# Kernel optimization log

Hardware: AMD Instinct MI355X
Metric: run time of the kernel (lower is better)

The kernel has to match this reference:

```python
import jax, jax.numpy as jnp
import numpy as np

TEMPERATURE = 2.0  # registered buffer in the torch module
TAU = 1.0
N_HEADS = 16


def setup_inputs() -> dict:
    key = jax.random.key(0)
    ks = jax.random.split(key, 8)
    B, S, D, N = 4, 1024, 1024, 4096
    scale = 1.0 / np.sqrt(D)
    return {
        "x": jax.random.normal(ks[0], (B, S, D), jnp.float32),
        "in_proj_w": jax.random.normal(ks[1], (3 * D, D), jnp.float32) * scale,
        "in_proj_b": jnp.zeros((3 * D,), jnp.float32),
        "out_w": jax.random.normal(ks[2], (D, D), jnp.float32) * scale,
        "out_b": jnp.zeros((D,), jnp.float32),
        "aff_w": jax.random.normal(ks[3], (N, D), jnp.float32) * scale,
        "aff_b": jnp.zeros((N,), jnp.float32),
        "k": 256,
    }


def _forward(x, in_proj_w, in_proj_b, out_w, out_b, aff_w, aff_b, k):
    B, S, D = x.shape
    H = N_HEADS
    hd = D // H
    # packed QKV projection (torch nn.MultiheadAttention layout)
    qkv = x @ in_proj_w.T + in_proj_b                      # [B,S,3D]
    q, kk, v = jnp.split(qkv, 3, axis=-1)
    q = q.reshape(B, S, H, hd).transpose(0, 2, 1, 3)       # [B,H,S,hd]
    kk = kk.reshape(B, S, H, hd).transpose(0, 2, 1, 3)
    v = v.reshape(B, S, H, hd).transpose(0, 2, 1, 3)
    scores = jnp.einsum("bhqd,bhkd->bhqk", q, kk) / np.sqrt(hd)
    attn = jax.nn.softmax(scores, axis=-1)                 # [B,H,S,S]
    ctx = jnp.einsum("bhqk,bhkd->bhqd", attn, v)
    ctx = ctx.transpose(0, 2, 1, 3).reshape(B, S, D)
    context = ctx @ out_w.T + out_b                        # [B,S,D]
    # neuron affinity -> max-pool over sequence
    affinity = context @ aff_w.T + aff_b                   # [B,S,N]
    pooled = affinity.max(axis=1)                          # [B,N]
    logits = pooled / TEMPERATURE
    # eval path of gumbel-softmax-topk: plain softmax(logits / tau)
    soft = jax.nn.softmax(logits / TAU, axis=-1)
    _, idx = jax.lax.top_k(logits, k)                      # [B,k]
    mask = jnp.zeros_like(soft).at[jnp.arange(soft.shape[0])[:, None], idx].set(1.0)
    masked = soft * mask
    weights = masked / (masked.sum(axis=-1, keepdims=True) + 1e-8)
    return idx, weights, context


def reference(x, in_proj_w, in_proj_b, out_w, out_b, aff_w, aff_b, k):
    return _forward(x, in_proj_w, in_proj_b, out_w, out_b, aff_w, aff_b, k)
```

## Files before the change

### kernel.cpp

```cpp
#include <hip/hip_runtime.h>
#include <math.h>

namespace {

constexpr int Bb = 4, Ss = 1024, Dd = 1024, Hh = 16, HDim = 64, Nn = 4096;
constexpr int Mm = Bb * Ss;

template <bool AFFMAX>
__global__ __launch_bounds__(256) void gemm_kernel(
    const float* __restrict__ A, const float* __restrict__ W,
    const float* __restrict__ bias, float* __restrict__ C, int K, int lda,
    int ldw, int ldc) {
  __shared__ float As[16][128];
  __shared__ float Ws[16][128];
  const int tid = threadIdx.x;
  const int tx = tid & 15, ty = tid >> 4;
  const int n0 = blockIdx.x * 128, m0 = blockIdx.y * 128;
  const int r = tid >> 1, kc = (tid & 1) * 8;
  const float* Arow = A + (size_t)(m0 + r) * lda + kc;
  const float* Wrow = W + (size_t)(n0 + r) * ldw + kc;
  float acc[8][8] = {};
  for (int kt = 0; kt < K; kt += 16) {
    float4 a0 = *(const float4*)(Arow + kt);
    float4 a1 = *(const float4*)(Arow + kt + 4);
    float4 w0 = *(const float4*)(Wrow + kt);
    float4 w1 = *(const float4*)(Wrow + kt + 4);
    __syncthreads();
    As[kc + 0][r] = a0.x; As[kc + 1][r] = a0.y;
    As[kc + 2][r] = a0.z; As[kc + 3][r] = a0.w;
    As[kc + 4][r] = a1.x; As[kc + 5][r] = a1.y;
    As[kc + 6][r] = a1.z; As[kc + 7][r] = a1.w;
    Ws[kc + 0][r] = w0.x; Ws[kc + 1][r] = w0.y;
    Ws[kc + 2][r] = w0.z; Ws[kc + 3][r] = w0.w;
    Ws[kc + 4][r] = w1.x; Ws[kc + 5][r] = w1.y;
    Ws[kc + 6][r] = w1.z; Ws[kc + 7][r] = w1.w;
    __syncthreads();
#pragma unroll
    for (int kk = 0; kk < 16; ++kk) {
      float4 a0r = *(const float4*)&As[kk][ty * 8];
      float4 a1r = *(const float4*)&As[kk][ty * 8 + 4];
      float4 b0r = *(const float4*)&Ws[kk][tx * 8];
      float4 b1r = *(const float4*)&Ws[kk][tx * 8 + 4];
      float av[8] = {a0r.x, a0r.y, a0r.z, a0r.w, a1r.x, a1r.y, a1r.z, a1r.w};
      float bv[8] = {b0r.x, b0r.y, b0r.z, b0r.w, b1r.x, b1r.y, b1r.z, b1r.w};
#pragma unroll
      for (int i = 0; i < 8; ++i)
#pragma unroll
        for (int j = 0; j < 8; ++j)
          acc[i][j] = fmaf(av[i], bv[j], acc[i][j]);
    }
  }
  if constexpr (!AFFMAX) {
#pragma unroll
    for (int i = 0; i < 8; ++i) {
      const int row = m0 + ty * 8 + i;
      float* crow = C + (size_t)row * ldc + n0 + tx * 8;
#pragma unroll
      for (int j = 0; j < 8; ++j) crow[j] = acc[i][j] + bias[n0 + tx * 8 + j];
    }
  } else {
    float cm[8];
#pragma unroll
    for (int j = 0; j < 8; ++j) {
      float m = acc[0][j];
#pragma unroll
      for (int i = 1; i < 8; ++i) m = fmaxf(m, acc[i][j]);
      cm[j] = m;
    }
    __syncthreads();
#pragma unroll
    for (int j = 0; j < 8; ++j) As[ty][tx * 8 + j] = cm[j];
    __syncthreads();
    if (tid < 128) {
      float m = As[0][tid];
#pragma unroll
      for (int yy = 1; yy < 16; ++yy) m = fmaxf(m, As[yy][tid]);
      C[(size_t)blockIdx.y * ldc + n0 + tid] = m;
    }
  }
}

__global__ __launch_bounds__(256) void attn_kernel(
    const float* __restrict__ qkv, float* __restrict__ ctx) {
  constexpr int LD = 68;
  __shared__ float Qs[64][LD];
  __shared__ float KPs[64][LD];
  __shared__ float Vs[64][LD];
  const int tid = threadIdx.x;
  const int tx = tid & 15, ty = tid >> 4;
  const int bh = blockIdx.y, b = bh >> 4, h = bh & 15;
  const int q0 = blockIdx.x * 64;
  const size_t rowstride = 3 * Dd;
  const float* qbase = qkv + (size_t)b * Ss * rowstride + h * HDim;
  const float* kbase = qbase + Dd;
  const float* vbase = qbase + 2 * Dd;
  {
    const int r = tid >> 2, c0 = (tid & 3) * 16;
    const float* qr = qbase + (size_t)(q0 + r) * rowstride + c0;
#pragma unroll
    for (int c = 0; c < 16; c += 4)
      *(float4*)&Qs[r][c0 + c] = *(const float4*)(qr + c);
  }
  float O[4][4] = {};
  float mrow[4] = {-INFINITY, -INFINITY, -INFINITY, -INFINITY};
  float lrow[4] = {};
  for (int kt0 = 0; kt0 < Ss; kt0 += 64) {
    const int r = tid >> 2, c0 = (tid & 3) * 16;
    const float* kr = kbase + (size_t)(kt0 + r) * rowstride + c0;
    const float* vr = vbase + (size_t)(kt0 + r) * rowstride + c0;
    float4 kv[4], vv[4];
#pragma unroll
    for (int c = 0; c < 4; ++c) {
      kv[c] = *(const float4*)(kr + c * 4);
      vv[c] = *(const float4*)(vr + c * 4);
    }
    __syncthreads();
#pragma unroll
    for (int c = 0; c < 4; ++c) {
      *(float4*)&Vs[r][c0 + 4 * c] = vv[c];
      KPs[c0 + 4 * c + 0][r] = kv[c].x;
      KPs[c0 + 4 * c + 1][r] = kv[c].y;
      KPs[c0 + 4 * c + 2][r] = kv[c].z;
      KPs[c0 + 4 * c + 3][r] = kv[c].w;
    }
    __syncthreads();
    float sc[4][4] = {};
#pragma unroll
    for (int d0 = 0; d0 < HDim; d0 += 4) {
      float4 qa[4];
#pragma unroll
      for (int i = 0; i < 4; ++i) qa[i] = *(const float4*)&Qs[ty * 4 + i][d0];
#pragma unroll
      for (int dd = 0; dd < 4; ++dd) {
        float4 kb = *(const float4*)&KPs[d0 + dd][tx * 4];
#pragma unroll
        for (int i = 0; i < 4; ++i) {
          float q = (dd == 0) ? qa[i].x : (dd == 1) ? qa[i].y
                    : (dd == 2) ? qa[i].z : qa[i].w;
          sc[i][0] = fmaf(q, kb.x, sc[i][0]);
          sc[i][1] = fmaf(q, kb.y, sc[i][1]);
          sc[i][2] = fmaf(q, kb.z, sc[i][2]);
          sc[i][3] = fmaf(q, kb.w, sc[i][3]);
        }
      }
    }
    __syncthreads();
#pragma unroll
    for (int i = 0; i < 4; ++i) {
      float s0 = sc[i][0] * 0.125f, s1 = sc[i][1] * 0.125f;
      float s2 = sc[i][2] * 0.125f, s3 = sc[i][3] * 0.125f;
      float tm = fmaxf(fmaxf(s0, s1), fmaxf(s2, s3));
#pragma unroll
      for (int msk = 1; msk < 16; msk <<= 1) tm = fmaxf(tm, __shfl_xor(tm, msk));
      float mnew = fmaxf(mrow[i], tm);
      float p0 = expf(s0 - mnew), p1 = expf(s1 - mnew);
      float p2 = expf(s2 - mnew), p3 = expf(s3 - mnew);
      KPs[ty * 4 + i][tx * 4 + 0] = p0;
      KPs[ty * 4 + i][tx * 4 + 1] = p1;
      KPs[ty * 4 + i][tx * 4 + 2] = p2;
      KPs[ty * 4 + i][tx * 4 + 3] = p3;
      float rs = p0 + p1 + p2 + p3;
#pragma unroll
      for (int msk = 1; msk < 16; msk <<= 1) rs += __shfl_xor(rs, msk);
      float corr = expf(mrow[i] - mnew);
      lrow[i] = lrow[i] * corr + rs;
      mrow[i] = mnew;
      O[i][0] *= corr; O[i][1] *= corr; O[i][2] *= corr; O[i][3] *= corr;
    }
    __syncthreads();
#pragma unroll
    for (int j0 = 0; j0 < 64; j0 += 4) {
      float4 pa[4];
#pragma unroll
      for (int i = 0; i < 4; ++i) pa[i] = *(const float4*)&KPs[ty * 4 + i][j0];
#pragma unroll
      for (int jj = 0; jj < 4; ++jj) {
        float4 vb = *(const float4*)&Vs[j0 + jj][tx * 4];
#pragma unroll
        for (int i = 0; i < 4; ++i) {
          float p = (jj == 0) ? pa[i].x : (jj == 1) ? pa[i].y
                    : (jj == 2) ? pa[i].z : pa[i].w;
          O[i][0] = fmaf(p, vb.x, O[i][0]);
          O[i][1] = fmaf(p, vb.y, O[i][1]);
          O[i][2] = fmaf(p, vb.z, O[i][2]);
          O[i][3] = fmaf(p, vb.w, O[i][3]);
        }
      }
    }
  }
#pragma unroll
  for (int i = 0; i < 4; ++i) {
    float inv = 1.0f / lrow[i];
    const int srow = q0 + ty * 4 + i;
    float* orow = ctx + ((size_t)(b * Ss + srow)) * Dd + h * HDim + tx * 4;
    orow[0] = O[i][0] * inv;
    orow[1] = O[i][1] * inv;
    orow[2] = O[i][2] * inv;
    orow[3] = O[i][3] * inv;
  }
}

__device__ inline unsigned int f2s(float f) {
  unsigned int u = __float_as_uint(f);
  return (u >> 31) ? ~u : (u | 0x80000000u);
}
__device__ inline float s2f(unsigned int s) {
  unsigned int u = (s >> 31) ? (s & 0x7fffffffu) : ~s;
  return __uint_as_float(u);
}

__global__ __launch_bounds__(256) void router_kernel(
    const float* __restrict__ partial, const float* __restrict__ aff_b,
    const int* __restrict__ kp, float* __restrict__ out, int out_size) {
  __shared__ unsigned long long keys[Nn];
  __shared__ float lorig[Nn];
  __shared__ float rv[4];
  const int tid = threadIdx.x;
  const int b = blockIdx.x;
  const int kcount = *kp;
  float* idx_out = out;
  float* w_out = out + (out_size - Mm * Dd - Bb * Nn);
  for (int n = tid; n < Nn; n += 256) {
    float m = partial[(size_t)(b * 8) * Nn + n];
#pragma unroll
    for (int t = 1; t < 8; ++t)
      m = fmaxf(m, partial[(size_t)(b * 8 + t) * Nn + n]);
    float lg = (m + aff_b[n]) * 0.5f;
    lorig[n] = lg;
    keys[n] = ((unsigned long long)f2s(lg) << 32) |
              (unsigned int)(Nn - 1 - n);
  }
  __syncthreads();
  for (int kk = 2; kk <= Nn; kk <<= 1) {
    for (int j = kk >> 1; j > 0; j >>= 1) {
#pragma unroll 4
      for (int t = tid; t < Nn / 2; t += 256) {
        const int i = 2 * j * (t / j) + (t % j);
        const int p = i + j;
        const bool desc = ((i & kk) == 0);
        unsigned long long a = keys[i], c = keys[p];
        if (desc ? (a < c) : (a > c)) { keys[i] = c; keys[p] = a; }
      }
      __syncthreads();
    }
  }
  const float gm = s2f((unsigned int)(keys[0] >> 32));
  float se = 0.f;
  for (int n = tid; n < Nn; n += 256) se += expf(lorig[n] - gm);
#pragma unroll
  for (int msk = 1; msk < 64; msk <<= 1) se += __shfl_xor(se, msk);
  if ((tid & 63) == 0) rv[tid >> 6] = se;
  __syncthreads();
  se = rv[0] + rv[1] + rv[2] + rv[3];
  __syncthreads();
  float es = 0.f;
  for (int p = tid; p < kcount; p += 256)
    es += expf(s2f((unsigned int)(keys[p] >> 32)) - gm);
#pragma unroll
  for (int msk = 1; msk < 64; msk <<= 1) es += __shfl_xor(es, msk);
  if ((tid & 63) == 0) rv[tid >> 6] = es;
  __syncthreads();
  es = rv[0] + rv[1] + rv[2] + rv[3];
  const float wd = es / se + 1e-8f;
  for (int n = tid; n < Nn; n += 256) w_out[(size_t)b * Nn + n] = 0.f;
  __syncthreads();
  for (int p = tid; p < kcount; p += 256) {
    const unsigned long long kkey = keys[p];
    const int n = Nn - 1 - (int)(kkey & 0xffffffffu);
    const float val = s2f((unsigned int)(kkey >> 32));
    idx_out[b * kcount + p] = (float)n;
    w_out[(size_t)b * Nn + n] = (expf(val - gm) / se) / wd;
  }
}

}

extern "C" void kernel_launch(void* const* d_in, const int* in_sizes, int n_in,
                              void* d_out, int out_size, void* d_ws,
                              size_t ws_size, hipStream_t stream) {
  (void)in_sizes; (void)n_in; (void)ws_size;
  const float* x = (const float*)d_in[0];
  const float* in_proj_w = (const float*)d_in[1];
  const float* in_proj_b = (const float*)d_in[2];
  const float* out_w = (const float*)d_in[3];
  const float* out_b = (const float*)d_in[4];
  const float* aff_w = (const float*)d_in[5];
  const float* aff_b = (const float*)d_in[6];
  const int* kp = (const int*)d_in[7];

  float* qkv = (float*)d_ws;
  float* ctxws = qkv + (size_t)Mm * 3 * Dd;
  float* partial = ctxws + (size_t)Mm * Dd;

  float* out = (float*)d_out;
  float* ctx_out = out + ((size_t)out_size - (size_t)Mm * Dd);

  gemm_kernel<false><<<dim3(3 * Dd / 128, Mm / 128), 256, 0, stream>>>(
      x, in_proj_w, in_proj_b, qkv, Dd, Dd, Dd, 3 * Dd);
  attn_kernel<<<dim3(Ss / 64, Bb * Hh), 256, 0, stream>>>(qkv, ctxws);
  gemm_kernel<false><<<dim3(Dd / 128, Mm / 128), 256, 0, stream>>>(
      ctxws, out_w, out_b, ctx_out, Dd, Dd, Dd, Dd);
  gemm_kernel<true><<<dim3(Nn / 128, Mm / 128), 256, 0, stream>>>(
      ctx_out, aff_w, nullptr, partial, Dd, Dd, Dd, Nn);
  router_kernel<<<dim3(Bb), 256, 0, stream>>>(partial, aff_b, kp, out, out_size);
}
```

Baseline: 1.287 ms.

## Double-buffer GEMM tiles, swizzle attention LDS, prefetch K/V, vectorize stores

The FP32 GEMM now keeps two shared-memory tile buffers, loads the next K slice into registers while the current one is computed, and maps threads to a warp-tiled layout. The max-pool epilogue reduces with shuffles, and bias/output writes use float4. The attention kernel XOR-swizzles its Q/K/V/P shared-memory indices to cut bank conflicts, prefetches the next K/V tile into registers, and switches to the fast __expf intrinsic. Together these aim to hide global-load latency and raise LDS throughput, at the cost of more registers and slightly less accurate exponentials.

```diff
diff --git a/kernel.cpp b/kernel.cpp
--- a/kernel.cpp
+++ b/kernel.cpp
@@ -6,43 +6,66 @@
 constexpr int Bb = 4, Ss = 1024, Dd = 1024, Hh = 16, HDim = 64, Nn = 4096;
 constexpr int Mm = Bb * Ss;
 
-template <bool AFFMAX>
-__global__ __launch_bounds__(256) void gemm_kernel(
+template <int MODE>
+__global__ __launch_bounds__(256, 4) void gemm_f32(
     const float* __restrict__ A, const float* __restrict__ W,
-    const float* __restrict__ bias, float* __restrict__ C, int K, int lda,
-    int ldw, int ldc) {
-  __shared__ float As[16][128];
-  __shared__ float Ws[16][128];
+    const float* __restrict__ bias, float* __restrict__ C, const int K,
+    const int ldc) {
+  __shared__ float As[2][16][128];
+  __shared__ float Ws[2][16][128];
   const int tid = threadIdx.x;
-  const int tx = tid & 15, ty = tid >> 4;
-  const int n0 = blockIdx.x * 128, m0 = blockIdx.y * 128;
-  const int r = tid >> 1, kc = (tid & 1) * 8;
-  const float* Arow = A + (size_t)(m0 + r) * lda + kc;
-  const float* Wrow = W + (size_t)(n0 + r) * ldw + kc;
+  const int lane = tid & 63, wv = tid >> 6;
+  const int wm = wv >> 1, wn = wv & 1;
+  const int lty = lane >> 3, ltx = lane & 7;
+  const int m0 = blockIdx.y * 128, n0 = blockIdx.x * 128;
+  const int row0 = wm * 64 + lty * 8;
+  const int col0 = wn * 64 + ltx * 8;
+  const int srow = tid >> 1, shalf = tid & 1;
+  const float* Ap = A + (size_t)(m0 + srow) * K + shalf * 8;
+  const float* Wp = W + (size_t)(n0 + srow) * K + shalf * 8;
+
+  float4 ar0 = *(const float4*)(Ap);
+  float4 ar1 = *(const float4*)(Ap + 4);
+  float4 wr0 = *(const float4*)(Wp);
+  float4 wr1 = *(const float4*)(Wp + 4);
+
   float acc[8][8] = {};
-  for (int kt = 0; kt < K; kt += 16) {
-    float4 a0 = *(const float4*)(Arow + kt);
-    float4 a1 = *(const float4*)(Arow + kt + 4);
-    float4 w0 = *(const float4*)(Wrow + kt);
-    float4 w1 = *(const float4*)(Wrow + kt + 4);
-    __syncthreads();
-    As[kc + 0][r] = a0.x; As[kc + 1][r] = a0.y;
-    As[kc + 2][r] = a0.z; As[kc + 3][r] = a0.w;
-    As[kc + 4][r] = a1.x; As[kc + 5][r] = a1.y;
-    As[kc + 6][r] = a1.z; As[kc + 7][r] = a1.w;
-    Ws[kc + 0][r] = w0.x; Ws[kc + 1][r] = w0.y;
-    Ws[kc + 2][r] = w0.z; Ws[kc + 3][r] = w0.w;
-    Ws[kc + 4][r] = w1.x; Ws[kc + 5][r] = w1.y;
-    Ws[kc + 6][r] = w1.z; Ws[kc + 7][r] = w1.w;
+  const int NT = K / 16;
+#pragma unroll 1
+  for (int kt = 0; kt < NT; ++kt) {
+    const int cb = kt & 1;
+    As[cb][shalf * 8 + 0][srow] = ar0.x;
+    As[cb][shalf * 8 + 1][srow] = ar0.y;
+    As[cb][shalf * 8 + 2][srow] = ar0.z;
+    As[cb][shalf * 8 + 3][srow] = ar0.w;
+    As[cb][shalf * 8 + 4][srow] = ar1.x;
+    As[cb][shalf * 8 + 5][srow] = ar1.y;
+    As[cb][shalf * 8 + 6][srow] = ar1.z;
+    As[cb][shalf * 8 + 7][srow] = ar1.w;
+    Ws[cb][shalf * 8 + 0][srow] = wr0.x;
+    Ws[cb][shalf * 8 + 1][srow] = wr0.y;
+    Ws[cb][shalf * 8 + 2][srow] = wr0.z;
+    Ws[cb][shalf * 8 + 3][srow] = wr0.w;
+    Ws[cb][shalf * 8 + 4][srow] = wr1.x;
+    Ws[cb][shalf * 8 + 5][srow] = wr1.y;
+    Ws[cb][shalf * 8 + 6][srow] = wr1.z;
+    Ws[cb][shalf * 8 + 7][srow] = wr1.w;
+    if (kt + 1 < NT) {
+      const int kb = (kt + 1) * 16;
+      ar0 = *(const float4*)(Ap + kb);
+      ar1 = *(const float4*)(Ap + kb + 4);
+      wr0 = *(const float4*)(Wp + kb);
+      wr1 = *(const float4*)(Wp + kb + 4);
+    }
     __syncthreads();
 #pragma unroll
     for (int kk = 0; kk < 16; ++kk) {
-      float4 a0r = *(const float4*)&As[kk][ty * 8];
-      float4 a1r = *(const float4*)&As[kk][ty * 8 + 4];
-      float4 b0r = *(const float4*)&Ws[kk][tx * 8];
-      float4 b1r = *(const float4*)&Ws[kk][tx * 8 + 4];
-      float av[8] = {a0r.x, a0r.y, a0r.z, a0r.w, a1r.x, a1r.y, a1r.z, a1r.w};
-      float bv[8] = {b0r.x, b0r.y, b0r.z, b0r.w, b1r.x, b1r.y, b1r.z, b1r.w};
+      float4 a0 = *(const float4*)&As[cb][kk][row0];
+      float4 a1 = *(const float4*)&As[cb][kk][row0 + 4];
+      float4 b0 = *(const float4*)&Ws[cb][kk][col0];
+      float4 b1 = *(const float4*)&Ws[cb][kk][col0 + 4];
+      float av[8] = {a0.x, a0.y, a0.z, a0.w, a1.x, a1.y, a1.z, a1.w};
+      float bv[8] = {b0.x, b0.y, b0.z, b0.w, b1.x, b1.y, b1.z, b1.w};
 #pragma unroll
       for (int i = 0; i < 8; ++i)
 #pragma unroll
@@ -50,13 +73,20 @@
           acc[i][j] = fmaf(av[i], bv[j], acc[i][j]);
     }
   }
-  if constexpr (!AFFMAX) {
+
+  if constexpr (MODE == 0) {
+    float4 bb0 = *(const float4*)&bias[n0 + col0];
+    float4 bb1 = *(const float4*)&bias[n0 + col0 + 4];
+    const float bv[8] = {bb0.x, bb0.y, bb0.z, bb0.w, bb1.x, bb1.y, bb1.z, bb1.w};
 #pragma unroll
     for (int i = 0; i < 8; ++i) {
-      const int row = m0 + ty * 8 + i;
-      float* crow = C + (size_t)row * ldc + n0 + tx * 8;
-#pragma unroll
-      for (int j = 0; j < 8; ++j) crow[j] = acc[i][j] + bias[n0 + tx * 8 + j];
+      float* crow = C + (size_t)(m0 + row0 + i) * ldc + n0 + col0;
+      float4 o0 = {acc[i][0] + bv[0], acc[i][1] + bv[1], acc[i][2] + bv[2],
+                   acc[i][3] + bv[3]};
+      float4 o1 = {acc[i][4] + bv[4], acc[i][5] + bv[5], acc[i][6] + bv[6],
+                   acc[i][7] + bv[7]};
+      *(float4*)(crow) = o0;
+      *(float4*)(crow + 4) = o1;
     }
   } else {
     float cm[8];
@@ -65,18 +95,22 @@
       float m = acc[0][j];
 #pragma unroll
       for (int i = 1; i < 8; ++i) m = fmaxf(m, acc[i][j]);
+      m = fmaxf(m, __shfl_xor(m, 8));
+      m = fmaxf(m, __shfl_xor(m, 16));
+      m = fmaxf(m, __shfl_xor(m, 32));
       cm[j] = m;
     }
     __syncthreads();
-#pragma unroll
-    for (int j = 0; j < 8; ++j) As[ty][tx * 8 + j] = cm[j];
-    __syncthreads();
-    if (tid < 128) {
-      float m = As[0][tid];
-#pragma unroll
-      for (int yy = 1; yy < 16; ++yy) m = fmaxf(m, As[yy][tid]);
-      C[(size_t)blockIdx.y * ldc + n0 + tid] = m;
-    }
+    float* buf = &As[0][0][0];
+    if (lty == 0) {
+      float4 c0v = {cm[0], cm[1], cm[2], cm[3]};
+      float4 c1v = {cm[4], cm[5], cm[6], cm[7]};
+      *(float4*)&buf[wm * 128 + col0] = c0v;
+      *(float4*)&buf[wm * 128 + col0 + 4] = c1v;
+    }
+    __syncthreads();
+    if (tid < 128)
+      C[(size_t)blockIdx.y * ldc + n0 + tid] = fmaxf(buf[tid], buf[128 + tid]);
   }
 }
 
@@ -88,51 +122,69 @@
   __shared__ float Vs[64][LD];
   const int tid = threadIdx.x;
   const int tx = tid & 15, ty = tid >> 4;
-  const int bh = blockIdx.y, b = bh >> 4, h = bh & 15;
+  const int b = blockIdx.y >> 4, h = blockIdx.y & 15;
   const int q0 = blockIdx.x * 64;
   const size_t rowstride = 3 * Dd;
   const float* qbase = qkv + (size_t)b * Ss * rowstride + h * HDim;
   const float* kbase = qbase + Dd;
   const float* vbase = qbase + 2 * Dd;
+  const int r = tid >> 2, c0 = (tid & 3) * 16;
+  const int rx = (r & 4) ? 16 : 0;
+  const int kx = (c0 & 32) ? 16 : 0;
   {
-    const int r = tid >> 2, c0 = (tid & 3) * 16;
     const float* qr = qbase + (size_t)(q0 + r) * rowstride + c0;
 #pragma unroll
     for (int c = 0; c < 16; c += 4)
-      *(float4*)&Qs[r][c0 + c] = *(const float4*)(qr + c);
+      *(float4*)&Qs[r][(c0 + c) ^ rx] = *(const float4*)(qr + c);
+  }
+  float4 kv[4], vv[4];
+  {
+    const float* kr = kbase + (size_t)r * rowstride + c0;
+    const float* vr = vbase + (size_t)r * rowstride + c0;
+#pragma unroll
+    for (int c = 0; c < 4; ++c) {
+      kv[c] = *(const float4*)(kr + 4 * c);
+      vv[c] = *(const float4*)(vr + 4 * c);
+    }
   }
   float O[4][4] = {};
   float mrow[4] = {-INFINITY, -INFINITY, -INFINITY, -INFINITY};
   float lrow[4] = {};
+  const int qkey = (ty & 1) ? 16 : 0;
+#pragma unroll 1
   for (int kt0 = 0; kt0 < Ss; kt0 += 64) {
-    const int r = tid >> 2, c0 = (tid & 3) * 16;
-    const float* kr = kbase + (size_t)(kt0 + r) * rowstride + c0;
-    const float* vr = vbase + (size_t)(kt0 + r) * rowstride + c0;
-    float4 kv[4], vv[4];
+    __syncthreads();
 #pragma unroll
     for (int c = 0; c < 4; ++c) {
-      kv[c] = *(const float4*)(kr + c * 4);
-      vv[c] = *(const float4*)(vr + c * 4);
-    }
-    __syncthreads();
-#pragma unroll
-    for (int c = 0; c < 4; ++c) {
-      *(float4*)&Vs[r][c0 + 4 * c] = vv[c];
-      KPs[c0 + 4 * c + 0][r] = kv[c].x;
-      KPs[c0 + 4 * c + 1][r] = kv[c].y;
-      KPs[c0 + 4 * c + 2][r] = kv[c].z;
-      KPs[c0 + 4 * c + 3][r] = kv[c].w;
-    }
-    __syncthreads();
+      *(float4*)&Vs[r][(c0 + 4 * c) ^ rx] = vv[c];
+      const int d = c0 + 4 * c;
+      const int cc = r ^ kx;
+      KPs[d + 0][cc] = kv[c].x;
+      KPs[d + 1][cc] = kv[c].y;
+      KPs[d + 2][cc] = kv[c].z;
+      KPs[d + 3][cc] = kv[c].w;
+    }
+    __syncthreads();
+    if (kt0 + 64 < Ss) {
+      const float* kr = kbase + (size_t)(kt0 + 64 + r) * rowstride + c0;
+      const float* vr = vbase + (size_t)(kt0 + 64 + r) * rowstride + c0;
+#pragma unroll
+      for (int c = 0; c < 4; ++c) {
+        kv[c] = *(const float4*)(kr + 4 * c);
+        vv[c] = *(const float4*)(vr + 4 * c);
+      }
+    }
     float sc[4][4] = {};
 #pragma unroll
     for (int d0 = 0; d0 < HDim; d0 += 4) {
+      const int kcol = (tx * 4) ^ ((d0 & 32) ? 16 : 0);
       float4 qa[4];
 #pragma unroll
-      for (int i = 0; i < 4; ++i) qa[i] = *(const float4*)&Qs[ty * 4 + i][d0];
+      for (int i = 0; i < 4; ++i)
+        qa[i] = *(const float4*)&Qs[ty * 4 + i][d0 ^ qkey];
 #pragma unroll
       for (int dd = 0; dd < 4; ++dd) {
-        float4 kb = *(const float4*)&KPs[d0 + dd][tx * 4];
+        float4 kb = *(const float4*)&KPs[d0 + dd][kcol];
 #pragma unroll
         for (int i = 0; i < 4; ++i) {
           float q = (dd == 0) ? qa[i].x : (dd == 1) ? qa[i].y
@@ -153,16 +205,14 @@
 #pragma unroll
       for (int msk = 1; msk < 16; msk <<= 1) tm = fmaxf(tm, __shfl_xor(tm, msk));
       float mnew = fmaxf(mrow[i], tm);
-      float p0 = expf(s0 - mnew), p1 = expf(s1 - mnew);
-      float p2 = expf(s2 - mnew), p3 = expf(s3 - mnew);
-      KPs[ty * 4 + i][tx * 4 + 0] = p0;
-      KPs[ty * 4 + i][tx * 4 + 1] = p1;
-      KPs[ty * 4 + i][tx * 4 + 2] = p2;
-      KPs[ty * 4 + i][tx * 4 + 3] = p3;
+      float p0 = __expf(s0 - mnew), p1 = __expf(s1 - mnew);
+      float p2 = __expf(s2 - mnew), p3 = __expf(s3 - mnew);
+      float4 pv4 = {p0, p1, p2, p3};
+      *(float4*)&KPs[ty * 4 + i][tx * 4] = pv4;
       float rs = p0 + p1 + p2 + p3;
 #pragma unroll
       for (int msk = 1; msk < 16; msk <<= 1) rs += __shfl_xor(rs, msk);
-      float corr = expf(mrow[i] - mnew);
+      float corr = __expf(mrow[i] - mnew);
       lrow[i] = lrow[i] * corr + rs;
       mrow[i] = mnew;
       O[i][0] *= corr; O[i][1] *= corr; O[i][2] *= corr; O[i][3] *= corr;
@@ -170,12 +220,13 @@
     __syncthreads();
 #pragma unroll
     for (int j0 = 0; j0 < 64; j0 += 4) {
+      const int vcol = (tx * 4) ^ ((j0 & 4) ? 16 : 0);
       float4 pa[4];
 #pragma unroll
       for (int i = 0; i < 4; ++i) pa[i] = *(const float4*)&KPs[ty * 4 + i][j0];
 #pragma unroll
       for (int jj = 0; jj < 4; ++jj) {
-        float4 vb = *(const float4*)&Vs[j0 + jj][tx * 4];
+        float4 vb = *(const float4*)&Vs[j0 + jj][vcol];
 #pragma unroll
         for (int i = 0; i < 4; ++i) {
           float p = (jj == 0) ? pa[i].x : (jj == 1) ? pa[i].y
@@ -192,11 +243,8 @@
   for (int i = 0; i < 4; ++i) {
     float inv = 1.0f / lrow[i];
     const int srow = q0 + ty * 4 + i;
-    float* orow = ctx + ((size_t)(b * Ss + srow)) * Dd + h * HDim + tx * 4;
-    orow[0] = O[i][0] * inv;
-    orow[1] = O[i][1] * inv;
-    orow[2] = O[i][2] * inv;
-    orow[3] = O[i][3] * inv;
+    float4 o = {O[i][0] * inv, O[i][1] * inv, O[i][2] * inv, O[i][3] * inv};
+    *(float4*)(ctx + ((size_t)(b * Ss + srow)) * Dd + h * HDim + tx * 4) = o;
   }
 }
 
@@ -227,8 +275,7 @@
       m = fmaxf(m, partial[(size_t)(b * 8 + t) * Nn + n]);
     float lg = (m + aff_b[n]) * 0.5f;
     lorig[n] = lg;
-    keys[n] = ((unsigned long long)f2s(lg) << 32) |
-              (unsigned int)(Nn - 1 - n);
+    keys[n] = ((unsigned long long)f2s(lg) << 32) | (unsigned int)(Nn - 1 - n);
   }
   __syncthreads();
   for (int kk = 2; kk <= Nn; kk <<= 1) {
@@ -295,12 +342,12 @@
   float* out = (float*)d_out;
   float* ctx_out = out + ((size_t)out_size - (size_t)Mm * Dd);
 
-  gemm_kernel<false><<<dim3(3 * Dd / 128, Mm / 128), 256, 0, stream>>>(
-      x, in_proj_w, in_proj_b, qkv, Dd, Dd, Dd, 3 * Dd);
+  gemm_f32<0><<<dim3(3 * Dd / 128, Mm / 128), 256, 0, stream>>>(
+      x, in_proj_w, in_proj_b, qkv, Dd, 3 * Dd);
   attn_kernel<<<dim3(Ss / 64, Bb * Hh), 256, 0, stream>>>(qkv, ctxws);
-  gemm_kernel<false><<<dim3(Dd / 128, Mm / 128), 256, 0, stream>>>(
-      ctxws, out_w, out_b, ctx_out, Dd, Dd, Dd, Dd);
-  gemm_kernel<true><<<dim3(Nn / 128, Mm / 128), 256, 0, stream>>>(
-      ctx_out, aff_w, nullptr, partial, Dd, Dd, Dd, Nn);
+  gemm_f32<0><<<dim3(Dd / 128, Mm / 128), 256, 0, stream>>>(
+      ctxws, out_w, out_b, ctx_out, Dd, Dd);
+  gemm_f32<2><<<dim3(Nn / 128, Mm / 128), 256, 0, stream>>>(
+      ctx_out, aff_w, nullptr, partial, Dd, Nn);
   router_kernel<<<dim3(Bb), 256, 0, stream>>>(partial, aff_b, kp, out, out_size);
 }
```

After: 1.409 ms. +9.5%, slower.

## Rework GEMM and attention kernels with larger per-thread tiles and prefetch

Applied to the files above, without the earlier changes.

The GEMMs move to 128-thread blocks with 16x8 or 8x8 per-thread tiles, register prefetch of the next K slice, vectorized stores and a wave-shuffle max reduction. The attention kernel is rewritten so each wave owns 64 query rows with 8x8 per-thread tiles, uses XOR-swizzled shared memory, prefetches K into registers, and loads V asynchronously with global_load_lds. It also switches to fast __expf. The aim is more FMA work per shared-memory load and less load latency. The cost is much higher register pressure and lower occupancy.

```diff
diff --git a/kernel.cpp b/kernel.cpp
--- a/kernel.cpp
+++ b/kernel.cpp
@@ -6,57 +6,102 @@
 constexpr int Bb = 4, Ss = 1024, Dd = 1024, Hh = 16, HDim = 64, Nn = 4096;
 constexpr int Mm = Bb * Ss;
 
-template <bool AFFMAX>
-__global__ __launch_bounds__(256) void gemm_kernel(
+template <int MODE, int TM>
+__global__ __launch_bounds__(128, 2) void gemm_f32(
     const float* __restrict__ A, const float* __restrict__ W,
-    const float* __restrict__ bias, float* __restrict__ C, int K, int lda,
-    int ldw, int ldc) {
-  __shared__ float As[16][128];
+    const float* __restrict__ bias, float* __restrict__ C, const int K,
+    const int ldc) {
+  constexpr int BM = TM * 8;
+  __shared__ float As[16][BM];
   __shared__ float Ws[16][128];
+  __shared__ float red[2][128];
   const int tid = threadIdx.x;
-  const int tx = tid & 15, ty = tid >> 4;
-  const int n0 = blockIdx.x * 128, m0 = blockIdx.y * 128;
-  const int r = tid >> 1, kc = (tid & 1) * 8;
-  const float* Arow = A + (size_t)(m0 + r) * lda + kc;
-  const float* Wrow = W + (size_t)(n0 + r) * ldw + kc;
-  float acc[8][8] = {};
-  for (int kt = 0; kt < K; kt += 16) {
-    float4 a0 = *(const float4*)(Arow + kt);
-    float4 a1 = *(const float4*)(Arow + kt + 4);
-    float4 w0 = *(const float4*)(Wrow + kt);
-    float4 w1 = *(const float4*)(Wrow + kt + 4);
-    __syncthreads();
-    As[kc + 0][r] = a0.x; As[kc + 1][r] = a0.y;
-    As[kc + 2][r] = a0.z; As[kc + 3][r] = a0.w;
-    As[kc + 4][r] = a1.x; As[kc + 5][r] = a1.y;
-    As[kc + 6][r] = a1.z; As[kc + 7][r] = a1.w;
-    Ws[kc + 0][r] = w0.x; Ws[kc + 1][r] = w0.y;
-    Ws[kc + 2][r] = w0.z; Ws[kc + 3][r] = w0.w;
-    Ws[kc + 4][r] = w1.x; Ws[kc + 5][r] = w1.y;
-    Ws[kc + 6][r] = w1.z; Ws[kc + 7][r] = w1.w;
-    __syncthreads();
+  const int rg = tid >> 4, cg = tid & 15;
+  const int m0 = blockIdx.y * BM, n0 = blockIdx.x * 128;
+
+  const int brow = tid;
+  int arow, ahalf;
+  if constexpr (TM == 16) { arow = tid; ahalf = 0; }
+  else { arow = tid >> 1; ahalf = (tid & 1) * 8; }
+  const float* Ap = A + (size_t)(m0 + arow) * K + ahalf;
+  const float* Wp = W + (size_t)(n0 + brow) * K;
+
+  float4 ar[4], br[4];
+  if constexpr (TM == 16) {
+#pragma unroll
+    for (int c = 0; c < 4; ++c) ar[c] = *(const float4*)(Ap + 4 * c);
+  } else {
+    ar[0] = *(const float4*)(Ap);
+    ar[1] = *(const float4*)(Ap + 4);
+  }
+#pragma unroll
+  for (int c = 0; c < 4; ++c) br[c] = *(const float4*)(Wp + 4 * c);
+
+  float acc[TM][8] = {};
+  const int NT = K / 16;
+#pragma unroll 1
+  for (int kt = 0; kt < NT; ++kt) {
+    __syncthreads();
+    {
+      const float* af = (const float*)ar;
+      const float* bf = (const float*)br;
+      if constexpr (TM == 16) {
+#pragma unroll
+        for (int c = 0; c < 16; ++c) As[c][arow] = af[c];
+      } else {
+#pragma unroll
+        for (int c = 0; c < 8; ++c) As[ahalf + c][arow] = af[c];
+      }
+#pragma unroll
+      for (int c = 0; c < 16; ++c) Ws[c][brow] = bf[c];
+    }
+    __syncthreads();
+    if (kt + 1 < NT) {
+      const int kb = (kt + 1) * 16;
+      if constexpr (TM == 16) {
+#pragma unroll
+        for (int c = 0; c < 4; ++c) ar[c] = *(const float4*)(Ap + kb + 4 * c);
+      } else {
+        ar[0] = *(const float4*)(Ap + kb);
+        ar[1] = *(const float4*)(Ap + kb + 4);
+      }
+#pragma unroll
+      for (int c = 0; c < 4; ++c) br[c] = *(const float4*)(Wp + kb + 4 * c);
+    }
 #pragma unroll
     for (int kk = 0; kk < 16; ++kk) {
-      float4 a0r = *(const float4*)&As[kk][ty * 8];
-      float4 a1r = *(const float4*)&As[kk][ty * 8 + 4];
-      float4 b0r = *(const float4*)&Ws[kk][tx * 8];
-      float4 b1r = *(const float4*)&Ws[kk][tx * 8 + 4];
-      float av[8] = {a0r.x, a0r.y, a0r.z, a0r.w, a1r.x, a1r.y, a1r.z, a1r.w};
-      float bv[8] = {b0r.x, b0r.y, b0r.z, b0r.w, b1r.x, b1r.y, b1r.z, b1r.w};
-#pragma unroll
-      for (int i = 0; i < 8; ++i)
+      float4 aq[TM / 4];
+      float4 bq[2];
+#pragma unroll
+      for (int s = 0; s < TM / 4; ++s)
+        aq[s] = *(const float4*)&As[kk][rg * TM + s * 4];
+      bq[0] = *(const float4*)&Ws[kk][cg * 8];
+      bq[1] = *(const float4*)&Ws[kk][cg * 8 + 4];
+      const float* av = (const float*)aq;
+      const float* bv = (const float*)bq;
+#pragma unroll
+      for (int i = 0; i < TM; ++i)
 #pragma unroll
         for (int j = 0; j < 8; ++j)
           acc[i][j] = fmaf(av[i], bv[j], acc[i][j]);
     }
   }
-  if constexpr (!AFFMAX) {
-#pragma unroll
-    for (int i = 0; i < 8; ++i) {
-      const int row = m0 + ty * 8 + i;
-      float* crow = C + (size_t)row * ldc + n0 + tx * 8;
-#pragma unroll
-      for (int j = 0; j < 8; ++j) crow[j] = acc[i][j] + bias[n0 + tx * 8 + j];
+
+  if constexpr (MODE == 0) {
+    float4 bb0 = *(const float4*)&bias[n0 + cg * 8];
+    float4 bb1 = *(const float4*)&bias[n0 + cg * 8 + 4];
+    const float* bv = (const float*)&bb0;
+    float bvv[8] = {bb0.x, bb0.y, bb0.z, bb0.w, bb1.x, bb1.y, bb1.z, bb1.w};
+    (void)bv;
+#pragma unroll
+    for (int i = 0; i < TM; ++i) {
+      float* crow = C + (size_t)(m0 + rg * TM + i) * ldc + n0 + cg * 8;
+      float4 o0 = {acc[i][0] + bvv[0], acc[i][1] + bvv[1],
+                   acc[i][2] + bvv[2], acc[i][3] + bvv[3]};
+      float4 o1 = {acc[i][4] + bvv[4], acc[i][5] + bvv[5],
+                   acc[i][6] + bvv[6], acc[i][7] + bvv[7]};
+      *(float4*)(crow) = o0;
+      *(float4*)(crow + 4) = o1;
     }
   } else {
     float cm[8];
@@ -64,139 +109,183 @@
     for (int j = 0; j < 8; ++j) {
       float m = acc[0][j];
 #pragma unroll
-      for (int i = 1; i < 8; ++i) m = fmaxf(m, acc[i][j]);
+      for (int i = 1; i < TM; ++i) m = fmaxf(m, acc[i][j]);
+      m = fmaxf(m, __shfl_xor(m, 16));
+      m = fmaxf(m, __shfl_xor(m, 32));
       cm[j] = m;
     }
-    __syncthreads();
-#pragma unroll
-    for (int j = 0; j < 8; ++j) As[ty][tx * 8 + j] = cm[j];
-    __syncthreads();
-    if (tid < 128) {
-      float m = As[0][tid];
-#pragma unroll
-      for (int yy = 1; yy < 16; ++yy) m = fmaxf(m, As[yy][tid]);
-      C[(size_t)blockIdx.y * ldc + n0 + tid] = m;
-    }
-  }
-}
-
-__global__ __launch_bounds__(256) void attn_kernel(
+    const int wv = tid >> 6;
+    if ((tid & 63) < 16) {
+      float4 c0 = {cm[0], cm[1], cm[2], cm[3]};
+      float4 c1 = {cm[4], cm[5], cm[6], cm[7]};
+      *(float4*)&red[wv][cg * 8] = c0;
+      *(float4*)&red[wv][cg * 8 + 4] = c1;
+    }
+    __syncthreads();
+    if (tid < 128)
+      C[(size_t)blockIdx.y * ldc + n0 + tid] =
+          fmaxf(red[0][tid], red[1][tid]);
+  }
+}
+
+__device__ __forceinline__ int sx(int r, int c) {
+  return c ^ ((((r >> 3) ^ r) & 7) << 3);
+}
+
+__global__ __launch_bounds__(128) void attn_kernel(
     const float* __restrict__ qkv, float* __restrict__ ctx) {
-  constexpr int LD = 68;
-  __shared__ float Qs[64][LD];
-  __shared__ float KPs[64][LD];
-  __shared__ float Vs[64][LD];
+  __shared__ float Qs[2][64][64];
+  __shared__ float Ks[64][64];
+  __shared__ float Ps1[64][64];
+  __shared__ float Vs[64][64];
   const int tid = threadIdx.x;
-  const int tx = tid & 15, ty = tid >> 4;
-  const int bh = blockIdx.y, b = bh >> 4, h = bh & 15;
-  const int q0 = blockIdx.x * 64;
-  const size_t rowstride = 3 * Dd;
-  const float* qbase = qkv + (size_t)b * Ss * rowstride + h * HDim;
-  const float* kbase = qbase + Dd;
-  const float* vbase = qbase + 2 * Dd;
+  const int wv = tid >> 6, lane = tid & 63;
+  const int rg = lane >> 3, cg = lane & 7;
+  const int b = blockIdx.y >> 4, h = blockIdx.y & 15;
+  const int q0 = blockIdx.x * 128 + wv * 64;
+  const size_t rstride = 3 * Dd;
+  const float* qb = qkv + (size_t)b * Ss * rstride + h * HDim;
+  const float* kb_ = qb + Dd;
+  const float* vb_ = qb + 2 * Dd;
+
   {
-    const int r = tid >> 2, c0 = (tid & 3) * 16;
-    const float* qr = qbase + (size_t)(q0 + r) * rowstride + c0;
-#pragma unroll
-    for (int c = 0; c < 16; c += 4)
-      *(float4*)&Qs[r][c0 + c] = *(const float4*)(qr + c);
-  }
-  float O[4][4] = {};
-  float mrow[4] = {-INFINITY, -INFINITY, -INFINITY, -INFINITY};
-  float lrow[4] = {};
-  for (int kt0 = 0; kt0 < Ss; kt0 += 64) {
-    const int r = tid >> 2, c0 = (tid & 3) * 16;
-    const float* kr = kbase + (size_t)(kt0 + r) * rowstride + c0;
-    const float* vr = vbase + (size_t)(kt0 + r) * rowstride + c0;
-    float4 kv[4], vv[4];
-#pragma unroll
-    for (int c = 0; c < 4; ++c) {
-      kv[c] = *(const float4*)(kr + c * 4);
-      vv[c] = *(const float4*)(vr + c * 4);
-    }
-    __syncthreads();
-#pragma unroll
-    for (int c = 0; c < 4; ++c) {
-      *(float4*)&Vs[r][c0 + 4 * c] = vv[c];
-      KPs[c0 + 4 * c + 0][r] = kv[c].x;
-      KPs[c0 + 4 * c + 1][r] = kv[c].y;
-      KPs[c0 + 4 * c + 2][r] = kv[c].z;
-      KPs[c0 + 4 * c + 3][r] = kv[c].w;
-    }
-    __syncthreads();
-    float sc[4][4] = {};
-#pragma unroll
+    const float* qr = qb + (size_t)(q0 + lane) * rstride;
+#pragma unroll
+    for (int c = 0; c < 64; c += 4)
+      *(float4*)&Qs[wv][lane][sx(lane, c)] = *(const float4*)(qr + c);
+  }
+  const int krow = tid >> 1, khalf = (tid & 1) * 32;
+  float4 kr[8];
+  {
+    const float* kp = kb_ + (size_t)krow * rstride + khalf;
+#pragma unroll
+    for (int c = 0; c < 8; ++c) kr[c] = *(const float4*)(kp + 4 * c);
+  }
+
+  float O[8][8] = {};
+  float mr[8], lr[8];
+#pragma unroll
+  for (int i = 0; i < 8; ++i) { mr[i] = -INFINITY; lr[i] = 0.f; }
+  float* Pw = (wv == 0) ? &Ks[0][0] : &Ps1[0][0];
+
+#pragma unroll 1
+  for (int kt = 0; kt < Ss; kt += 64) {
+    __syncthreads();
+#pragma unroll
+    for (int c = 0; c < 8; ++c)
+      *(float4*)&Ks[krow][sx(krow, khalf + 4 * c)] = kr[c];
+    __syncthreads();
+#pragma unroll
+    for (int j = 0; j < 8; ++j) {
+      const int r0 = wv * 32 + j * 4;
+      const int r = r0 + (lane >> 4);
+      const int c = ((lane & 15) * 4) ^ ((((r >> 3) ^ r) & 7) << 3);
+      const float* src = vb_ + (size_t)(kt + r) * rstride + c;
+      float* dst = &Vs[r0][0];
+      __builtin_amdgcn_global_load_lds(
+          (const __attribute__((address_space(1))) void*)src,
+          (__attribute__((address_space(3))) void*)dst, 16, 0, 0);
+    }
+    if (kt + 64 < Ss) {
+      const float* kp = kb_ + (size_t)(kt + 64 + krow) * rstride + khalf;
+#pragma unroll
+      for (int c = 0; c < 8; ++c) kr[c] = *(const float4*)(kp + 4 * c);
+    }
+    float sc[8][8] = {};
+#pragma unroll 2
     for (int d0 = 0; d0 < HDim; d0 += 4) {
-      float4 qa[4];
-#pragma unroll
-      for (int i = 0; i < 4; ++i) qa[i] = *(const float4*)&Qs[ty * 4 + i][d0];
-#pragma unroll
-      for (int dd = 0; dd < 4; ++dd) {
-        float4 kb = *(const float4*)&KPs[d0 + dd][tx * 4];
-#pragma unroll
-        for (int i = 0; i < 4; ++i) {
-          float q = (dd == 0) ? qa[i].x : (dd == 1) ? qa[i].y
-                    : (dd == 2) ? qa[i].z : qa[i].w;
-          sc[i][0] = fmaf(q, kb.x, sc[i][0]);
-          sc[i][1] = fmaf(q, kb.y, sc[i][1]);
-          sc[i][2] = fmaf(q, kb.z, sc[i][2]);
-          sc[i][3] = fmaf(q, kb.w, sc[i][3]);
+      float4 qa[8], kv[8];
+#pragma unroll
+      for (int i = 0; i < 8; ++i) {
+        const int r = rg * 8 + i;
+        qa[i] = *(const float4*)&Qs[wv][r][sx(r, d0)];
+      }
+#pragma unroll
+      for (int j = 0; j < 8; ++j) {
+        const int r = cg * 8 + j;
+        kv[j] = *(const float4*)&Ks[r][sx(r, d0)];
+      }
+#pragma unroll
+      for (int i = 0; i < 8; ++i)
+#pragma unroll
+        for (int j = 0; j < 8; ++j) {
+          sc[i][j] = fmaf(qa[i].x, kv[j].x, sc[i][j]);
+          sc[i][j] = fmaf(qa[i].y, kv[j].y, sc[i][j]);
+          sc[i][j] = fmaf(qa[i].z, kv[j].z, sc[i][j]);
+          sc[i][j] = fmaf(qa[i].w, kv[j].w, sc[i][j]);
         }
-      }
-    }
-    __syncthreads();
-#pragma unroll
-    for (int i = 0; i < 4; ++i) {
-      float s0 = sc[i][0] * 0.125f, s1 = sc[i][1] * 0.125f;
-      float s2 = sc[i][2] * 0.125f, s3 = sc[i][3] * 0.125f;
-      float tm = fmaxf(fmaxf(s0, s1), fmaxf(s2, s3));
-#pragma unroll
-      for (int msk = 1; msk < 16; msk <<= 1) tm = fmaxf(tm, __shfl_xor(tm, msk));
-      float mnew = fmaxf(mrow[i], tm);
-      float p0 = expf(s0 - mnew), p1 = expf(s1 - mnew);
-      float p2 = expf(s2 - mnew), p3 = expf(s3 - mnew);
-      KPs[ty * 4 + i][tx * 4 + 0] = p0;
-      KPs[ty * 4 + i][tx * 4 + 1] = p1;
-      KPs[ty * 4 + i][tx * 4 + 2] = p2;
-      KPs[ty * 4 + i][tx * 4 + 3] = p3;
-      float rs = p0 + p1 + p2 + p3;
-#pragma unroll
-      for (int msk = 1; msk < 16; msk <<= 1) rs += __shfl_xor(rs, msk);
-      float corr = expf(mrow[i] - mnew);
-      lrow[i] = lrow[i] * corr + rs;
-      mrow[i] = mnew;
-      O[i][0] *= corr; O[i][1] *= corr; O[i][2] *= corr; O[i][3] *= corr;
-    }
-    __syncthreads();
-#pragma unroll
+    }
+    __syncthreads();
+#pragma unroll
+    for (int i = 0; i < 8; ++i) {
+      float sv[8];
+#pragma unroll
+      for (int j = 0; j < 8; ++j) sv[j] = sc[i][j] * 0.125f;
+      float tm = sv[0];
+#pragma unroll
+      for (int j = 1; j < 8; ++j) tm = fmaxf(tm, sv[j]);
+      tm = fmaxf(tm, __shfl_xor(tm, 1));
+      tm = fmaxf(tm, __shfl_xor(tm, 2));
+      tm = fmaxf(tm, __shfl_xor(tm, 4));
+      const float mnew = fmaxf(mr[i], tm);
+      float p[8];
+      float rs = 0.f;
+#pragma unroll
+      for (int j = 0; j < 8; ++j) { p[j] = __expf(sv[j] - mnew); rs += p[j]; }
+      rs += __shfl_xor(rs, 1);
+      rs += __shfl_xor(rs, 2);
+      rs += __shfl_xor(rs, 4);
+      const float corr = __expf(mr[i] - mnew);
+      lr[i] = lr[i] * corr + rs;
+      mr[i] = mnew;
+#pragma unroll
+      for (int c = 0; c < 8; ++c) O[i][c] *= corr;
+      const int r = rg * 8 + i;
+      float* pp = &Pw[r * 64 + sx(r, cg * 8)];
+      float4 p0 = {p[0], p[1], p[2], p[3]};
+      float4 p1 = {p[4], p[5], p[6], p[7]};
+      *(float4*)pp = p0;
+      *(float4*)(pp + 4) = p1;
+    }
+#pragma unroll 2
     for (int j0 = 0; j0 < 64; j0 += 4) {
-      float4 pa[4];
-#pragma unroll
-      for (int i = 0; i < 4; ++i) pa[i] = *(const float4*)&KPs[ty * 4 + i][j0];
+      float4 pa[8];
+#pragma unroll
+      for (int i = 0; i < 8; ++i) {
+        const int r = rg * 8 + i;
+        pa[i] = *(const float4*)&Pw[r * 64 + sx(r, j0)];
+      }
 #pragma unroll
       for (int jj = 0; jj < 4; ++jj) {
-        float4 vb = *(const float4*)&Vs[j0 + jj][tx * 4];
-#pragma unroll
-        for (int i = 0; i < 4; ++i) {
-          float p = (jj == 0) ? pa[i].x : (jj == 1) ? pa[i].y
-                    : (jj == 2) ? pa[i].z : pa[i].w;
-          O[i][0] = fmaf(p, vb.x, O[i][0]);
-          O[i][1] = fmaf(p, vb.y, O[i][1]);
-          O[i][2] = fmaf(p, vb.z, O[i][2]);
-          O[i][3] = fmaf(p, vb.w, O[i][3]);
+        const int vr = j0 + jj;
+        const float4 v0 = *(const float4*)&Vs[vr][sx(vr, cg * 8)];
+        const float4 v1 = *(const float4*)&Vs[vr][sx(vr, cg * 8) + 4];
+#pragma unroll
+        for (int i = 0; i < 8; ++i) {
+          const float p = (jj == 0) ? pa[i].x
+                          : (jj == 1) ? pa[i].y
+                          : (jj == 2) ? pa[i].z : pa[i].w;
+          O[i][0] = fmaf(p, v0.x, O[i][0]);
+          O[i][1] = fmaf(p, v0.y, O[i][1]);
+          O[i][2] = fmaf(p, v0.z, O[i][2]);
+          O[i][3] = fmaf(p, v0.w, O[i][3]);
+          O[i][4] = fmaf(p, v1.x, O[i][4]);
+          O[i][5] = fmaf(p, v1.y, O[i][5]);
+          O[i][6] = fmaf(p, v1.z, O[i][6]);
+          O[i][7] = fmaf(p, v1.w, O[i][7]);
         }
       }
     }
   }
 #pragma unroll
-  for (int i = 0; i < 4; ++i) {
-    float inv = 1.0f / lrow[i];
-    const int srow = q0 + ty * 4 + i;
-    float* orow = ctx + ((size_t)(b * Ss + srow)) * Dd + h * HDim + tx * 4;
-    orow[0] = O[i][0] * inv;
-    orow[1] = O[i][1] * inv;
-    orow[2] = O[i][2] * inv;
-    orow[3] = O[i][3] * inv;
+  for (int i = 0; i < 8; ++i) {
+    const float inv = 1.0f / lr[i];
+    float* orow =
+        ctx + ((size_t)(b * Ss + q0 + rg * 8 + i)) * Dd + h * HDim + cg * 8;
+    float4 o0 = {O[i][0] * inv, O[i][1] * inv, O[i][2] * inv, O[i][3] * inv};
+    float4 o1 = {O[i][4] * inv, O[i][5] * inv, O[i][6] * inv, O[i][7] * inv};
+    *(float4*)(orow) = o0;
+    *(float4*)(orow + 4) = o1;
   }
 }
 
@@ -227,8 +316,7 @@
       m = fmaxf(m, partial[(size_t)(b * 8 + t) * Nn + n]);
     float lg = (m + aff_b[n]) * 0.5f;
     lorig[n] = lg;
-    keys[n] = ((unsigned long long)f2s(lg) << 32) |
-              (unsigned int)(Nn - 1 - n);
+    keys[n] = ((unsigned long long)f2s(lg) << 32) | (unsigned int)(Nn - 1 - n);
   }
   __syncthreads();
   for (int kk = 2; kk <= Nn; kk <<= 1) {
@@ -295,12 +383,12 @@
   float* out = (float*)d_out;
   float* ctx_out = out + ((size_t)out_size - (size_t)Mm * Dd);
 
-  gemm_kernel<false><<<dim3(3 * Dd / 128, Mm / 128), 256, 0, stream>>>(
-      x, in_proj_w, in_proj_b, qkv, Dd, Dd, Dd, 3 * Dd);
-  attn_kernel<<<dim3(Ss / 64, Bb * Hh), 256, 0, stream>>>(qkv, ctxws);
-  gemm_kernel<false><<<dim3(Dd / 128, Mm / 128), 256, 0, stream>>>(
-      ctxws, out_w, out_b, ctx_out, Dd, Dd, Dd, Dd);
-  gemm_kernel<true><<<dim3(Nn / 128, Mm / 128), 256, 0, stream>>>(
-      ctx_out, aff_w, nullptr, partial, Dd, Dd, Dd, Nn);
+  gemm_f32<0, 16><<<dim3(3 * Dd / 128, Mm / 128), 128, 0, stream>>>(
+      x, in_proj_w, in_proj_b, qkv, Dd, 3 * Dd);
+  attn_kernel<<<dim3(Ss / 128, Bb * Hh), 128, 0, stream>>>(qkv, ctxws);
+  gemm_f32<0, 8><<<dim3(Dd / 128, Mm / 64), 128, 0, stream>>>(
+      ctxws, out_w, out_b, ctx_out, Dd, Dd);
+  gemm_f32<2, 16><<<dim3(Nn / 128, Mm / 128), 128, 0, stream>>>(
+      ctx_out, aff_w, nullptr, partial, Dd, Nn);
   router_kernel<<<dim3(Bb), 256, 0, stream>>>(partial, aff_b, kp, out, out_size);
 }
```

Result: slower. 2.858 ms (+122.0%).
